# Kernel optimization log

Measured on AMD Instinct MI355X. Metric: run time of the kernel, lower is better.

The kernel has to match this reference:

```python
import jax, jax.numpy as jnp
import numpy as np

L_IN, L_ENC, B = 1024, 1024, 16
D_IN, D_ENC, D_EMB = 512, 512, 512


def setup_inputs() -> dict:
    key = jax.random.key(0)
    ks = jax.random.split(key, 9)
    s_in = 1.0 / np.sqrt(D_IN)
    s_emb = 1.0 / np.sqrt(D_EMB)
    s_enc = 1.0 / np.sqrt(D_ENC)
    return {
        "in_seq": jax.random.normal(ks[0], (L_IN, B, D_IN), jnp.float32),
        "enc_seq": jax.random.normal(ks[1], (L_ENC, B, D_ENC), jnp.float32),
        "prev_target_seq": jax.random.normal(ks[2], (L_IN, B, D_EMB), jnp.float32),
        # torch Linear weights: (out_features, in_features)
        "W_in2enc": jax.random.normal(ks[3], (D_ENC, D_IN), jnp.float32) * s_in,
        "b_in2enc": jnp.zeros((D_ENC,), jnp.float32),
        "W_lab2enc": jax.random.normal(ks[4], (D_ENC, D_EMB), jnp.float32) * s_emb,
        "b_lab2enc": jnp.zeros((D_ENC,), jnp.float32),
        "W_enc2in": jax.random.normal(ks[5], (D_IN, D_ENC), jnp.float32) * s_enc,
        "b_enc2in": jnp.zeros((D_IN,), jnp.float32),
    }


def reference(in_seq, enc_seq, prev_target_seq,
              W_in2enc, b_in2enc, W_lab2enc, b_lab2enc, W_enc2in, b_enc2in):
    # d_vals: (L_in, B, D_enc) = proj(in_seq) + proj(prev_target_seq)
    in_proj = jnp.einsum('lbi,ei->lbe', in_seq, W_in2enc) + b_in2enc
    tgt_proj = jnp.einsum('lbm,em->lbe', prev_target_seq, W_lab2enc) + b_lab2enc
    d_vals = in_proj + tgt_proj
    # raw attention scores: (L_in, L_enc, B) dot products over D_enc
    scores = jnp.einsum('lbe,mbe->lmb', d_vals, enc_seq)
    # sum-normalization (NOT softmax) over the encoder-length axis
    attn = scores / jnp.sum(scores, axis=1, keepdims=True)
    # weighted sum of encoder states: (L_in, B, D_enc)
    context = jnp.einsum('lmb,mbe->lbe', attn, enc_seq)
    # project back to input dim
    return jnp.einsum('lbe,ie->lbi', context, W_enc2in) + b_enc2in
```

## Files before the change

kernel.cpp:

```cpp
#include <hip/hip_runtime.h>
#include <cstdint>

static constexpr int LDR = 8192;

typedef uint16_t u16;
typedef __attribute__((ext_vector_type(8))) short short8;
typedef __attribute__((ext_vector_type(4))) float f32x4;
struct alignas(8) U16x4 { u16 x, y, z, w; };

__device__ __forceinline__ u16 f2bf(float f) {
    union { float f; unsigned u; } v; v.f = f;
    unsigned r = v.u + 0x7fffu + ((v.u >> 16) & 1u);
    return (u16)(r >> 16);
}

__device__ __forceinline__ short8 cvt8(const float4 a, const float4 b) {
    short8 r;
    r[0]=(short)f2bf(a.x); r[1]=(short)f2bf(a.y); r[2]=(short)f2bf(a.z); r[3]=(short)f2bf(a.w);
    r[4]=(short)f2bf(b.x); r[5]=(short)f2bf(b.y); r[6]=(short)f2bf(b.z); r[7]=(short)f2bf(b.w);
    return r;
}

__device__ __forceinline__ void gl_lds16(const u16* g, unsigned ldsaddr) {
    asm volatile("s_mov_b32 m0, %0\n\t"
                 "global_load_lds_dwordx4 %1, off"
                 :: "s"(__builtin_amdgcn_readfirstlane(ldsaddr)), "v"(g)
                 : "memory");
}

template<int MODE>
__global__ __launch_bounds__(256) void gemm_async(
    const u16* __restrict__ A, const u16* __restrict__ Bm,
    const float* __restrict__ b1, const float* __restrict__ b2,
    const float* __restrict__ b3, const float* __restrict__ Sinv,
    u16* __restrict__ Cb, float* __restrict__ Cf)
{
    constexpr int K   = (MODE == 1 || MODE == 5) ? 1024 : 512;
    constexpr int BM  = (MODE == 5 || MODE == 6) ? 64 : 128;
    constexpr int NJ  = (BM == 128) ? 4 : 2;
    constexpr int NIA = BM / 32;
    constexpr int NIB = 4;
    constexpr int ASZ = BM * 128;
    constexpr int BSZ = 128 * 128;
    constexpr int LDA = (MODE == 1 || MODE == 5) ? 1024 : 512;
    constexpr int LDB = (MODE == 1 || MODE == 5) ? 1024 : 512;

    __shared__ __align__(16) u16 lds[(2*ASZ + 2*BSZ) / 2];

    const int z    = blockIdx.z;
    const int row0 = blockIdx.y * BM;
    const int col0 = blockIdx.x * 128;
    if constexpr (MODE == 5) {
        if (row0 >= col0 + 128) return;
    }
    const int tid  = threadIdx.x;
    const int l    = tid & 63, w = tid >> 6;
    const int wm   = (BM == 128) ? (w >> 1) : 0;
    const int wn   = (BM == 128) ? (w & 1) : w;
    const int quad = l >> 4, l16 = l & 15;

    const u16* Ab = A;
    const u16* Bb = Bm;
    if constexpr (MODE == 5) { Ab = A + z*524288; Bb = Bm + z*524288; }
    if constexpr (MODE == 6) { Bb = Bm + z*262144; }
    if constexpr (MODE == 4) { Ab = A + z*524288; Bb = Bm + z*262144; }

    const int lq = l >> 3;
    const int loffu = ((l & 7) ^ lq) * 8;
    const u16* gA[NIA];
    #pragma unroll
    for (int i = 0; i < NIA; ++i)
        gA[i] = Ab + (size_t)(row0 + i*32 + w*8 + lq) * LDA + loffu;
    const u16* gB[NIB];
    #pragma unroll
    for (int i = 0; i < NIB; ++i)
        gB[i] = Bb + (size_t)(col0 + i*32 + w*8 + lq) * LDB + loffu;

    const unsigned lbase = (unsigned)(size_t)&lds[0];

    auto stage = [&](int c) {
        #pragma unroll
        for (int i = 0; i < NIA; ++i) {
            gl_lds16(gA[i], lbase + c*ASZ + i*4096 + w*1024);
            gA[i] += 64;
        }
        #pragma unroll
        for (int i = 0; i < NIB; ++i) {
            gl_lds16(gB[i], lbase + 2*ASZ + c*BSZ + i*4096 + w*1024);
            gB[i] += 64;
        }
    };

    f32x4 acc[4][NJ] = {};
    const int swzr = (l16 & 7) << 3;
    const int arow = wm * 64;
    const int brow = wn * (BM == 128 ? 64 : 32);

    stage(0);
    int cur = 0;
    for (int kb = 0; kb < K; kb += 64) {
        asm volatile("s_waitcnt vmcnt(0)" ::: "memory");
        __syncthreads();
        if (kb + 64 < K) stage(cur ^ 1);
        const int abase = cur * (ASZ/2);
        const int bbase = ASZ + cur * (BSZ/2);
        #pragma unroll
        for (int kk = 0; kk < 2; ++kk) {
            const int koff = (kk*32 + quad*8) ^ swzr;
            short8 af[4], bfr[NJ];
            #pragma unroll
            for (int i = 0; i < 4; ++i)
                af[i] = *(const short8*)&lds[abase + (arow + i*16 + l16)*64 + koff];
            #pragma unroll
            for (int j = 0; j < NJ; ++j)
                bfr[j] = *(const short8*)&lds[bbase + (brow + j*16 + l16)*64 + koff];
            #pragma unroll
            for (int i = 0; i < 4; ++i)
                #pragma unroll
                for (int j = 0; j < NJ; ++j)
                    acc[i][j] = __builtin_amdgcn_mfma_f32_16x16x32_bf16(af[i], bfr[j], acc[i][j], 0, 0, 0);
        }
        cur ^= 1;
    }

    #pragma unroll
    for (int i = 0; i < 4; ++i) {
        const int grow = row0 + arow + i*16 + quad*4;
        #pragma unroll
        for (int j = 0; j < NJ; ++j) {
            const int gcol = col0 + brow + j*16 + l16;
            #pragma unroll
            for (int r = 0; r < 4; ++r) {
                float v = acc[i][j][r];
                const int R = grow + r;
                if constexpr (MODE == 1) {
                    v += b1[gcol] + b2[gcol];
                    Cb[((R & 15)*1024 + (R >> 4))*512 + gcol] = f2bf(v);
                } else if constexpr (MODE == 5) {
                    const u16 o = f2bf(v);
                    Cb[z*262144 + R*512 + gcol] = o;
                    Cb[z*262144 + gcol*512 + R] = o;
                } else if constexpr (MODE == 6) {
                    Cb[z*262144 + R*512 + gcol] = f2bf(v);
                } else {
                    const float s = Sinv[R*16 + z];
                    Cf[(R*16 + z)*512 + gcol] = v * s + b3[gcol];
                }
            }
        }
    }
}

__global__ __launch_bounds__(256) void enct_kernel(
    const float* __restrict__ E, u16* __restrict__ EncT, double* __restrict__ part)
{
    __shared__ float tile[64][65];
    __shared__ double sred[256];
    const int bb = blockIdx.z;
    const int m0 = blockIdx.y * 64;
    const int e0 = blockIdx.x * 64;
    const int t = threadIdx.x;
    const int tr = t >> 4;
    const int tc4 = (t & 15) * 4;
    #pragma unroll
    for (int it = 0; it < 4; ++it) {
        const int ml = tr + it*16;
        float4 v = *(const float4*)&E[(m0+ml)*LDR + bb*512 + e0 + tc4];
        *(float4*)&tile[ml][tc4] = v;
    }
    __syncthreads();
    #pragma unroll
    for (int it = 0; it < 4; ++it) {
        const int el = tr + it*16;
        U16x4 o;
        o.x = f2bf(tile[tc4+0][el]);
        o.y = f2bf(tile[tc4+1][el]);
        o.z = f2bf(tile[tc4+2][el]);
        o.w = f2bf(tile[tc4+3][el]);
        *(U16x4*)&EncT[bb*524288 + (e0+el)*1024 + m0 + tc4] = o;
    }
    const int el = t & 63, mq = t >> 6;
    double a = 0.0;
    #pragma unroll
    for (int j = 0; j < 16; ++j) a += (double)tile[mq*16 + j][el];
    sred[t] = a;
    __syncthreads();
    if (t < 64) {
        double s = sred[t] + sred[t+64] + sred[t+128] + sred[t+192];
        part[blockIdx.y*8192 + bb*512 + e0 + t] = s;
    }
}

__global__ __launch_bounds__(256) void prep_small(
    const float* __restrict__ W1, const float* __restrict__ W2,
    const float* __restrict__ W3, const float* __restrict__ b1,
    const float* __restrict__ b2, const double* __restrict__ part,
    u16* __restrict__ W12, u16* __restrict__ W3b,
    double* __restrict__ u, double* __restrict__ cd)
{
    const int blk = blockIdx.x, tid = threadIdx.x;
    if (blk < 384) {
        const int idx = blk*256 + tid;
        if (idx < 65536) {
            const int r = idx >> 7, k8 = (idx & 127) * 8;
            const float* src = (k8 < 512) ? (W1 + r*512 + k8) : (W2 + r*512 + (k8 - 512));
            float4 a = *(const float4*)src;
            float4 b = *((const float4*)src + 1);
            *(short8*)&W12[r*1024 + k8] = cvt8(a, b);
        } else {
            const int i2 = idx - 65536;
            const int r = i2 >> 6, k8 = (i2 & 63) * 8;
            const float* src = W3 + r*512 + k8;
            float4 a = *(const float4*)src;
            float4 b = *((const float4*)src + 1);
            *(short8*)&W3b[r*512 + k8] = cvt8(a, b);
        }
        return;
    }
    __shared__ double es_l[512];
    __shared__ double red[256];
    int b;
    if (blk < 448) b = ((blk - 384) & 31) >> 1;
    else           b = blk - 448;
    for (int e = tid; e < 512; e += 256) {
        double s = 0.0;
        #pragma unroll
        for (int c = 0; c < 16; ++c) s += part[c*8192 + b*512 + e];
        es_l[e] = s;
    }
    __syncthreads();
    if (blk < 448) {
        const int blk2 = blk - 384;
        const int which = blk2 >> 5;
        const int t = (blk2 & 31)*256 + tid;
        const int i = t & 511;
        const float* W = which ? W2 : W1;
        double a = 0.0;
        for (int e = 0; e < 512; ++e) a += (double)W[e*512 + i] * es_l[e];
        u[which*8192 + t] = a;
    } else {
        double a = 0.0;
        for (int e = tid; e < 512; e += 256) a += (double)(b1[e] + b2[e]) * es_l[e];
        red[tid] = a; __syncthreads();
        for (int s = 128; s > 0; s >>= 1) { if (tid < s) red[tid] += red[tid+s]; __syncthreads(); }
        if (tid == 0) cd[b] = red[0];
    }
}

__global__ __launch_bounds__(256) void s_xt_kernel(
    const float* __restrict__ X, const float* __restrict__ T,
    const double* __restrict__ u, const double* __restrict__ cd,
    float* __restrict__ Sinv, u16* __restrict__ XT)
{
    const int wave = threadIdx.x >> 6, lane = threadIdx.x & 63;
    const int b = blockIdx.x & 15, g = blockIdx.x >> 4;
    const int e = lane * 8;
    double u1r[8], u2r[8];
    #pragma unroll
    for (int k = 0; k < 8; ++k) {
        u1r[k] = u[b*512 + e + k];
        u2r[k] = u[8192 + b*512 + e + k];
    }
    const double cb = cd[b];
    #pragma unroll 2
    for (int i = 0; i < 8; ++i) {
        const int j = g*32 + wave*8 + i;
        const int r = j*16 + b;
        float4 x0 = *(const float4*)&X[r*512 + e];
        float4 x1 = *(const float4*)&X[r*512 + e + 4];
        float4 t0 = *(const float4*)&T[r*512 + e];
        float4 t1 = *(const float4*)&T[r*512 + e + 4];
        double a = 0.0;
        a += (double)x0.x*u1r[0] + (double)x0.y*u1r[1] + (double)x0.z*u1r[2] + (double)x0.w*u1r[3];
        a += (double)x1.x*u1r[4] + (double)x1.y*u1r[5] + (double)x1.z*u1r[6] + (double)x1.w*u1r[7];
        a += (double)t0.x*u2r[0] + (double)t0.y*u2r[1] + (double)t0.z*u2r[2] + (double)t0.w*u2r[3];
        a += (double)t1.x*u2r[4] + (double)t1.y*u2r[5] + (double)t1.z*u2r[6] + (double)t1.w*u2r[7];
        *(short8*)&XT[r*1024 + e]       = cvt8(x0, x1);
        *(short8*)&XT[r*1024 + 512 + e] = cvt8(t0, t1);
        #pragma unroll
        for (int off = 32; off > 0; off >>= 1) a += __shfl_down(a, off, 64);
        if (lane == 0) Sinv[r] = (float)(1.0 / (a + cb));
    }
}

extern "C" void kernel_launch(void* const* d_in, const int* in_sizes, int n_in,
                              void* d_out, int out_size, void* d_ws, size_t ws_size,
                              hipStream_t stream)
{
    const float* X   = (const float*)d_in[0];
    const float* Enc = (const float*)d_in[1];
    const float* T   = (const float*)d_in[2];
    const float* W1  = (const float*)d_in[3];
    const float* b1  = (const float*)d_in[4];
    const float* W2  = (const float*)d_in[5];
    const float* b2  = (const float*)d_in[6];
    const float* W3  = (const float*)d_in[7];
    const float* b3  = (const float*)d_in[8];
    float* out = (float*)d_out;

    char* w = (char*)d_ws;
    u16*    dvals_g  = (u16*)(w);
    u16*    EncT_bf  = (u16*)(w + 16777216);
    u16*    Gram_bf  = (u16*)(w + 33554432);
    u16*    HT_bf    = (u16*)(w + 41943040);
    u16*    W12      = (u16*)(w + 50331648);
    u16*    W3b      = (u16*)(w + 51380224);
    double* part     = (double*)(w + 51904512);
    double* u        = (double*)(w + 52953088);
    double* cd       = (double*)(w + 53084160);
    float*  Sinv     = (float*)(w + 53084288);
    u16*    XTb      = (u16*)d_out;

    dim3 blk(256);
    enct_kernel <<<dim3(8, 16, 16), blk, 0, stream>>>(Enc, EncT_bf, part);
    prep_small  <<<dim3(464),       blk, 0, stream>>>(W1, W2, W3, b1, b2, part, W12, W3b, u, cd);
    s_xt_kernel <<<dim3(512),       blk, 0, stream>>>(X, T, u, cd, Sinv, XTb);

    gemm_async<5><<<dim3(4, 8, 16),  blk, 0, stream>>>(EncT_bf, EncT_bf, b1, b2, b3, Sinv, Gram_bf, out);
    gemm_async<6><<<dim3(4, 8, 16),  blk, 0, stream>>>(W3b, Gram_bf, b1, b2, b3, Sinv, HT_bf, out);
    gemm_async<1><<<dim3(4, 128, 1), blk, 0, stream>>>(XTb, W12, b1, b2, b3, Sinv, dvals_g, out);
    gemm_async<4><<<dim3(4, 8, 16),  blk, 0, stream>>>(dvals_g, HT_bf, b1, b2, b3, Sinv, dvals_g, out);
}
```

Baseline: 251.0 us.

## Merge independent stages into shared launches and compute full Gram without mirroring

Independent work is packed into combined grids to cut launch count from seven to five and let unrelated stages fill the device together. The Enc transpose runs with the weight bf16 conversion, the S/XT pass with the Gram GEMM, and the input projection GEMM with the W3·Gram GEMM. The Gram GEMM no longer skips lower-triangle tiles or writes a mirrored copy: every tile is computed and stored once, trading extra MFMA work for simpler, coalesced stores. LDS is now dynamic, so the lightweight S/XT blocks in the merged grid also reserve the GEMM's shared memory, which may limit occupancy.

New measurement: 241.6 us. -3.7%, faster.

```diff
diff --git a/kernel.cpp b/kernel.cpp
--- a/kernel.cpp
+++ b/kernel.cpp
@@ -29,10 +29,11 @@
 }
 
 template<int MODE>
-__global__ __launch_bounds__(256) void gemm_async(
+__device__ __forceinline__ void gemm_body(
+    int bx, int by, int z,
     const u16* __restrict__ A, const u16* __restrict__ Bm,
-    const float* __restrict__ b1, const float* __restrict__ b2,
-    const float* __restrict__ b3, const float* __restrict__ Sinv,
+    const float* __restrict__ b1v, const float* __restrict__ b2v,
+    const float* __restrict__ b3v, const float* __restrict__ Sinv,
     u16* __restrict__ Cb, float* __restrict__ Cf)
 {
     constexpr int K   = (MODE == 1 || MODE == 5) ? 1024 : 512;
@@ -45,14 +46,10 @@
     constexpr int LDA = (MODE == 1 || MODE == 5) ? 1024 : 512;
     constexpr int LDB = (MODE == 1 || MODE == 5) ? 1024 : 512;
 
-    __shared__ __align__(16) u16 lds[(2*ASZ + 2*BSZ) / 2];
-
-    const int z    = blockIdx.z;
-    const int row0 = blockIdx.y * BM;
-    const int col0 = blockIdx.x * 128;
-    if constexpr (MODE == 5) {
-        if (row0 >= col0 + 128) return;
-    }
+    extern __shared__ __align__(16) u16 lds[];
+
+    const int row0 = by * BM;
+    const int col0 = bx * 128;
     const int tid  = threadIdx.x;
     const int l    = tid & 63, w = tid >> 6;
     const int wm   = (BM == 128) ? (w >> 1) : 0;
@@ -134,126 +131,26 @@
                 float v = acc[i][j][r];
                 const int R = grow + r;
                 if constexpr (MODE == 1) {
-                    v += b1[gcol] + b2[gcol];
+                    v += b1v[gcol] + b2v[gcol];
                     Cb[((R & 15)*1024 + (R >> 4))*512 + gcol] = f2bf(v);
-                } else if constexpr (MODE == 5) {
-                    const u16 o = f2bf(v);
-                    Cb[z*262144 + R*512 + gcol] = o;
-                    Cb[z*262144 + gcol*512 + R] = o;
-                } else if constexpr (MODE == 6) {
+                } else if constexpr (MODE == 5 || MODE == 6) {
                     Cb[z*262144 + R*512 + gcol] = f2bf(v);
                 } else {
                     const float s = Sinv[R*16 + z];
-                    Cf[(R*16 + z)*512 + gcol] = v * s + b3[gcol];
+                    Cf[(R*16 + z)*512 + gcol] = v * s + b3v[gcol];
                 }
             }
         }
     }
 }
 
-__global__ __launch_bounds__(256) void enct_kernel(
-    const float* __restrict__ E, u16* __restrict__ EncT, double* __restrict__ part)
-{
-    __shared__ float tile[64][65];
-    __shared__ double sred[256];
-    const int bb = blockIdx.z;
-    const int m0 = blockIdx.y * 64;
-    const int e0 = blockIdx.x * 64;
-    const int t = threadIdx.x;
-    const int tr = t >> 4;
-    const int tc4 = (t & 15) * 4;
-    #pragma unroll
-    for (int it = 0; it < 4; ++it) {
-        const int ml = tr + it*16;
-        float4 v = *(const float4*)&E[(m0+ml)*LDR + bb*512 + e0 + tc4];
-        *(float4*)&tile[ml][tc4] = v;
-    }
-    __syncthreads();
-    #pragma unroll
-    for (int it = 0; it < 4; ++it) {
-        const int el = tr + it*16;
-        U16x4 o;
-        o.x = f2bf(tile[tc4+0][el]);
-        o.y = f2bf(tile[tc4+1][el]);
-        o.z = f2bf(tile[tc4+2][el]);
-        o.w = f2bf(tile[tc4+3][el]);
-        *(U16x4*)&EncT[bb*524288 + (e0+el)*1024 + m0 + tc4] = o;
-    }
-    const int el = t & 63, mq = t >> 6;
-    double a = 0.0;
-    #pragma unroll
-    for (int j = 0; j < 16; ++j) a += (double)tile[mq*16 + j][el];
-    sred[t] = a;
-    __syncthreads();
-    if (t < 64) {
-        double s = sred[t] + sred[t+64] + sred[t+128] + sred[t+192];
-        part[blockIdx.y*8192 + bb*512 + e0 + t] = s;
-    }
-}
-
-__global__ __launch_bounds__(256) void prep_small(
-    const float* __restrict__ W1, const float* __restrict__ W2,
-    const float* __restrict__ W3, const float* __restrict__ b1,
-    const float* __restrict__ b2, const double* __restrict__ part,
-    u16* __restrict__ W12, u16* __restrict__ W3b,
-    double* __restrict__ u, double* __restrict__ cd)
-{
-    const int blk = blockIdx.x, tid = threadIdx.x;
-    if (blk < 384) {
-        const int idx = blk*256 + tid;
-        if (idx < 65536) {
-            const int r = idx >> 7, k8 = (idx & 127) * 8;
-            const float* src = (k8 < 512) ? (W1 + r*512 + k8) : (W2 + r*512 + (k8 - 512));
-            float4 a = *(const float4*)src;
-            float4 b = *((const float4*)src + 1);
-            *(short8*)&W12[r*1024 + k8] = cvt8(a, b);
-        } else {
-            const int i2 = idx - 65536;
-            const int r = i2 >> 6, k8 = (i2 & 63) * 8;
-            const float* src = W3 + r*512 + k8;
-            float4 a = *(const float4*)src;
-            float4 b = *((const float4*)src + 1);
-            *(short8*)&W3b[r*512 + k8] = cvt8(a, b);
-        }
-        return;
-    }
-    __shared__ double es_l[512];
-    __shared__ double red[256];
-    int b;
-    if (blk < 448) b = ((blk - 384) & 31) >> 1;
-    else           b = blk - 448;
-    for (int e = tid; e < 512; e += 256) {
-        double s = 0.0;
-        #pragma unroll
-        for (int c = 0; c < 16; ++c) s += part[c*8192 + b*512 + e];
-        es_l[e] = s;
-    }
-    __syncthreads();
-    if (blk < 448) {
-        const int blk2 = blk - 384;
-        const int which = blk2 >> 5;
-        const int t = (blk2 & 31)*256 + tid;
-        const int i = t & 511;
-        const float* W = which ? W2 : W1;
-        double a = 0.0;
-        for (int e = 0; e < 512; ++e) a += (double)W[e*512 + i] * es_l[e];
-        u[which*8192 + t] = a;
-    } else {
-        double a = 0.0;
-        for (int e = tid; e < 512; e += 256) a += (double)(b1[e] + b2[e]) * es_l[e];
-        red[tid] = a; __syncthreads();
-        for (int s = 128; s > 0; s >>= 1) { if (tid < s) red[tid] += red[tid+s]; __syncthreads(); }
-        if (tid == 0) cd[b] = red[0];
-    }
-}
-
-__global__ __launch_bounds__(256) void s_xt_kernel(
-    const float* __restrict__ X, const float* __restrict__ T,
+__device__ __forceinline__ void s_xt_body(
+    int bid, const float* __restrict__ X, const float* __restrict__ T,
     const double* __restrict__ u, const double* __restrict__ cd,
     float* __restrict__ Sinv, u16* __restrict__ XT)
 {
     const int wave = threadIdx.x >> 6, lane = threadIdx.x & 63;
-    const int b = blockIdx.x & 15, g = blockIdx.x >> 4;
+    const int b = bid & 15, g = bid >> 4;
     const int e = lane * 8;
     double u1r[8], u2r[8];
     #pragma unroll
@@ -283,6 +180,146 @@
     }
 }
 
+__global__ __launch_bounds__(256) void enct_wconv(
+    const float* __restrict__ E, u16* __restrict__ EncT, double* __restrict__ part,
+    const float* __restrict__ W1, const float* __restrict__ W2,
+    const float* __restrict__ W3, u16* __restrict__ W12, u16* __restrict__ W3b)
+{
+    const int bid = blockIdx.x, t = threadIdx.x;
+    if (bid >= 2048) {
+        const int idx = (bid - 2048)*256 + t;
+        if (idx < 65536) {
+            const int r = idx >> 7, k8 = (idx & 127) * 8;
+            const float* src = (k8 < 512) ? (W1 + r*512 + k8) : (W2 + r*512 + (k8 - 512));
+            float4 a = *(const float4*)src;
+            float4 b = *((const float4*)src + 1);
+            *(short8*)&W12[r*1024 + k8] = cvt8(a, b);
+        } else {
+            const int i2 = idx - 65536;
+            const int r = i2 >> 6, k8 = (i2 & 63) * 8;
+            const float* src = W3 + r*512 + k8;
+            float4 a = *(const float4*)src;
+            float4 b = *((const float4*)src + 1);
+            *(short8*)&W3b[r*512 + k8] = cvt8(a, b);
+        }
+        return;
+    }
+    __shared__ float tile[64][65];
+    __shared__ double sred[256];
+    const int ex = bid & 7;
+    const int my = (bid >> 3) & 15;
+    const int bb = bid >> 7;
+    const int m0 = my * 64;
+    const int e0 = ex * 64;
+    const int tr = t >> 4;
+    const int tc4 = (t & 15) * 4;
+    #pragma unroll
+    for (int it = 0; it < 4; ++it) {
+        const int ml = tr + it*16;
+        float4 v = *(const float4*)&E[(m0+ml)*LDR + bb*512 + e0 + tc4];
+        *(float4*)&tile[ml][tc4] = v;
+    }
+    __syncthreads();
+    #pragma unroll
+    for (int it = 0; it < 4; ++it) {
+        const int el = tr + it*16;
+        U16x4 o;
+        o.x = f2bf(tile[tc4+0][el]);
+        o.y = f2bf(tile[tc4+1][el]);
+        o.z = f2bf(tile[tc4+2][el]);
+        o.w = f2bf(tile[tc4+3][el]);
+        *(U16x4*)&EncT[bb*524288 + (e0+el)*1024 + m0 + tc4] = o;
+    }
+    const int el = t & 63, mq = t >> 6;
+    double a = 0.0;
+    #pragma unroll
+    for (int j = 0; j < 16; ++j) a += (double)tile[mq*16 + j][el];
+    sred[t] = a;
+    __syncthreads();
+    if (t < 64) {
+        double s = sred[t] + sred[t+64] + sred[t+128] + sred[t+192];
+        part[my*8192 + bb*512 + e0 + t] = s;
+    }
+}
+
+__global__ __launch_bounds__(256) void prep80(
+    const float* __restrict__ W1, const float* __restrict__ W2,
+    const float* __restrict__ b1, const float* __restrict__ b2,
+    const double* __restrict__ part, double* __restrict__ u, double* __restrict__ cd)
+{
+    const int blk = blockIdx.x, tid = threadIdx.x;
+    __shared__ double es_l[512];
+    __shared__ double red[256];
+    int b;
+    if (blk < 64) b = (blk & 31) >> 1;
+    else          b = blk - 64;
+    for (int e = tid; e < 512; e += 256) {
+        double s = 0.0;
+        #pragma unroll
+        for (int c = 0; c < 16; ++c) s += part[c*8192 + b*512 + e];
+        es_l[e] = s;
+    }
+    __syncthreads();
+    if (blk < 64) {
+        const int which = blk >> 5;
+        const int t = (blk & 31)*256 + tid;
+        const int i = t & 511;
+        const float* W = which ? W2 : W1;
+        double a = 0.0;
+        for (int e = 0; e < 512; ++e) a += (double)W[e*512 + i] * es_l[e];
+        u[which*8192 + t] = a;
+    } else {
+        double a = 0.0;
+        for (int e = tid; e < 512; e += 256) a += (double)(b1[e] + b2[e]) * es_l[e];
+        red[tid] = a; __syncthreads();
+        for (int s = 128; s > 0; s >>= 1) { if (tid < s) red[tid] += red[tid+s]; __syncthreads(); }
+        if (tid == 0) cd[b] = red[0];
+    }
+}
+
+__global__ __launch_bounds__(256) void fused_a(
+    const float* __restrict__ X, const float* __restrict__ T,
+    const double* __restrict__ u, const double* __restrict__ cd,
+    float* __restrict__ Sinv, u16* __restrict__ XT,
+    const u16* __restrict__ EncT, u16* __restrict__ Gram)
+{
+    const int bid = blockIdx.x;
+    if (bid < 512) {
+        s_xt_body(bid, X, T, u, cd, Sinv, XT);
+    } else {
+        const int idx = bid - 512;
+        gemm_body<5>(idx & 3, (idx >> 2) & 7, idx >> 5,
+                     EncT, EncT, nullptr, nullptr, nullptr, nullptr, Gram, nullptr);
+    }
+}
+
+__global__ __launch_bounds__(256) void fused_b(
+    const u16* __restrict__ XT, const u16* __restrict__ W12,
+    const float* __restrict__ b1, const float* __restrict__ b2,
+    u16* __restrict__ dvals_g,
+    const u16* __restrict__ W3b, const u16* __restrict__ Gram,
+    u16* __restrict__ HT)
+{
+    const int bid = blockIdx.x;
+    if (bid < 512) {
+        gemm_body<1>(bid & 3, bid >> 2, 0,
+                     XT, W12, b1, b2, nullptr, nullptr, dvals_g, nullptr);
+    } else {
+        const int idx = bid - 512;
+        gemm_body<6>(idx & 3, (idx >> 2) & 7, idx >> 5,
+                     W3b, Gram, nullptr, nullptr, nullptr, nullptr, HT, nullptr);
+    }
+}
+
+__global__ __launch_bounds__(256) void gemm_m4(
+    const u16* __restrict__ dvals_g, const u16* __restrict__ HT,
+    const float* __restrict__ b3, const float* __restrict__ Sinv,
+    float* __restrict__ out)
+{
+    gemm_body<4>(blockIdx.x, blockIdx.y, blockIdx.z,
+                 dvals_g, HT, nullptr, nullptr, b3, Sinv, nullptr, out);
+}
+
 extern "C" void kernel_launch(void* const* d_in, const int* in_sizes, int n_in,
                               void* d_out, int out_size, void* d_ws, size_t ws_size,
                               hipStream_t stream)
@@ -312,12 +349,9 @@
     u16*    XTb      = (u16*)d_out;
 
     dim3 blk(256);
-    enct_kernel <<<dim3(8, 16, 16), blk, 0, stream>>>(Enc, EncT_bf, part);
-    prep_small  <<<dim3(464),       blk, 0, stream>>>(W1, W2, W3, b1, b2, part, W12, W3b, u, cd);
-    s_xt_kernel <<<dim3(512),       blk, 0, stream>>>(X, T, u, cd, Sinv, XTb);
-
-    gemm_async<5><<<dim3(4, 8, 16),  blk, 0, stream>>>(EncT_bf, EncT_bf, b1, b2, b3, Sinv, Gram_bf, out);
-    gemm_async<6><<<dim3(4, 8, 16),  blk, 0, stream>>>(W3b, Gram_bf, b1, b2, b3, Sinv, HT_bf, out);
-    gemm_async<1><<<dim3(4, 128, 1), blk, 0, stream>>>(XTb, W12, b1, b2, b3, Sinv, dvals_g, out);
-    gemm_async<4><<<dim3(4, 8, 16),  blk, 0, stream>>>(dvals_g, HT_bf, b1, b2, b3, Sinv, dvals_g, out);
-}
+    enct_wconv <<<dim3(2432), blk, 0, stream>>>(Enc, EncT_bf, part, W1, W2, W3, W12, W3b);
+    prep80     <<<dim3(80),   blk, 0, stream>>>(W1, W2, b1, b2, part, u, cd);
+    fused_a    <<<dim3(1024), blk, 49152, stream>>>(X, T, u, cd, Sinv, XTb, EncT_bf, Gram_bf);
+    fused_b    <<<dim3(1024), blk, 65536, stream>>>(XTb, W12, b1, b2, dvals_g, W3b, Gram_bf, HT_bf);
+    gemm_m4    <<<dim3(4, 8, 16), blk, 65536, stream>>>(dvals_g, HT_bf, b3, Sinv, out);
+}
```
